# Optimization experiments

Measured on AMD Instinct MI355X. Metric: run time of the kernel, lower is better.

## Reference

```python
import jax, jax.numpy as jnp
import numpy as np

KR = 2  # nb_row == stride_row
KC = 2  # nb_col == stride_col


def setup_inputs() -> dict:
    key = jax.random.key(0)
    k1, k2, k3 = jax.random.split(key, 3)
    B, C, H, W_ = 32, 32, 128, 128
    F = 64
    OR, OC = H // KR, W_ // KC
    x = jax.random.normal(k1, (B, C, H, W_), dtype=jnp.float32)
    W = jax.random.normal(k2, (F, C, H, W_), dtype=jnp.float32) * 0.05
    b = jax.random.normal(k3, (OR, OC, F), dtype=jnp.float32) * 0.05
    return {"x": x, "W": W, "b": b}


def reference(x, W, b):
    # x: (B, C, H, W), W: (F, C, H, W) -- unshared per-pixel weights
    # per-pixel channel contraction: (B, F, H, W)
    out = jnp.einsum('bchw,fchw->bfhw', x, W)
    B, F, H, Wd = out.shape
    OR, OC = H // KR, Wd // KC
    # stride*avg_pool == exact sum over non-overlapping (KR, KC) patches
    out = out.reshape(B, F, OR, KR, OC, KC).sum(axis=(3, 5))
    # keras does a RAW reshape of b from (OR, OC, F) to (1, F, OR, OC)
    out = out + b.reshape(1, F, OR, OC)
    return jax.nn.relu(out)
```

## Files before the change

kernel.cpp:

```cpp
#include <hip/hip_runtime.h>
#include <stdint.h>


#define CC  32
#define HH  128
#define WWD 128
#define FF  64
#define ORR 64
#define OCC 64
#define NIT 32
#define HW  (HH * WWD)
#define CHW (CC * HH * WWD)

__global__ __launch_bounds__(512, 4) void lc2d_kernel(
    const float* __restrict__ x, const float* __restrict__ wgt,
    const float* __restrict__ bias, float* __restrict__ out)
{
    __shared__ __align__(16) float Xs[4][2048];
    __shared__ __align__(16) float Ws[4][2048];

    const int tid  = threadIdx.x;
    const int id   = blockIdx.x;
    const int fblk = id >> 8;
    const int low  = id & 255;
    const int oct = ((low & 1) << 1) | (low >> 7);
    const int orr = (low >> 1) & 63;
    const int w0  = oct * 32;
    const int h0  = orr * 2;

    const int lane = tid & 63;
    const int wv   = tid >> 6;
    const int chk  = lane & 7;
    const int sub  = lane >> 3;

    const int r  = wv * 8 + sub;
    const int sr = r >> 5;
    const int br = r & 31;
    const float* gx = x   + (((br * CC) * HH) + h0 + sr) * WWD + w0 + chk * 4;
    const float* gw = wgt + ((((fblk * 32 + br) * CC) * HH) + h0 + sr) * WWD + w0 + chk * 4;

    auto issue = [&](int p) {
        __builtin_amdgcn_global_load_lds(
            (const __attribute__((address_space(1))) void*)gx,
            (__attribute__((address_space(3))) void*)(&Xs[p][wv * 256]), 16, 0, 0);
        __builtin_amdgcn_global_load_lds(
            (const __attribute__((address_space(1))) void*)gw,
            (__attribute__((address_space(3))) void*)(&Ws[p][wv * 256]), 16, 0, 0);
        gx += HW; gw += HW;
    };

    const int ocg = tid & 7;
    const int bg  = (tid >> 3) & 7;
    const int xoff = bg * 128 + ocg * 4;
    const int woff = wv * 128 + ocg * 4;

    float acc0[4][4], acc1[4][4];
#pragma unroll
    for (int i = 0; i < 4; ++i)
#pragma unroll
        for (int q = 0; q < 4; ++q) { acc0[i][q] = 0.f; acc1[i][q] = 0.f; }

    issue(0); issue(1); issue(2); issue(3);

    for (int it = 0; it < NIT; ++it) {
        const int rem = NIT - 1 - it;
        if (rem >= 3)      asm volatile("s_waitcnt vmcnt(6)");
        else if (rem == 2) asm volatile("s_waitcnt vmcnt(4)");
        else if (rem == 1) asm volatile("s_waitcnt vmcnt(2)");
        else               asm volatile("s_waitcnt vmcnt(0)");
        __builtin_amdgcn_sched_barrier(0);
        __builtin_amdgcn_s_barrier();
        __builtin_amdgcn_sched_barrier(0);

        const int p = it & 3;
        const float* Xp = Xs[p];
        const float* Wp = Ws[p];
#pragma unroll
        for (int s = 0; s < 2; ++s) {
            const float4* xr = (const float4*)(Xp + s * 1024 + xoff);
            const float4* wr = (const float4*)(Wp + s * 1024 + woff);
            float4 xa[4], wb[4];
#pragma unroll
            for (int i = 0; i < 4; ++i) xa[i] = xr[i * 8];
#pragma unroll
            for (int q = 0; q < 4; ++q) wb[q] = wr[q * 8];
#pragma unroll
            for (int i = 0; i < 4; ++i)
#pragma unroll
                for (int q = 0; q < 4; ++q) {
                    acc0[i][q] = fmaf(xa[i].x, wb[q].x, acc0[i][q]);
                    acc0[i][q] = fmaf(xa[i].y, wb[q].y, acc0[i][q]);
                    acc1[i][q] = fmaf(xa[i].z, wb[q].z, acc1[i][q]);
                    acc1[i][q] = fmaf(xa[i].w, wb[q].w, acc1[i][q]);
                }
        }
        __builtin_amdgcn_sched_barrier(0);
        __builtin_amdgcn_s_barrier();
        __builtin_amdgcn_sched_barrier(0);
        if (it + 4 < NIT) issue(p);
    }

    const int oc0 = oct * 16 + ocg * 2;
#pragma unroll
    for (int q = 0; q < 4; ++q) {
        const int f = fblk * 32 + wv * 4 + q;
        const float2 bv = *(const float2*)(bias + f * (ORR * OCC) + orr * OCC + oc0);
#pragma unroll
        for (int i = 0; i < 4; ++i) {
            const int b = bg * 4 + i;
            float2 o;
            o.x = fmaxf(acc0[i][q] + bv.x, 0.f);
            o.y = fmaxf(acc1[i][q] + bv.y, 0.f);
            *(float2*)(out + (((b * FF + f) * ORR + orr) * OCC) + oc0) = o;
        }
    }
}

extern "C" void kernel_launch(void* const* d_in, const int* in_sizes, int n_in,
                              void* d_out, int out_size, void* d_ws, size_t ws_size,
                              hipStream_t stream) {
    (void)in_sizes; (void)n_in; (void)d_ws; (void)ws_size; (void)out_size;
    const float* x    = (const float*)d_in[0];
    const float* wgt  = (const float*)d_in[1];
    const float* bias = (const float*)d_in[2];
    float* out        = (float*)d_out;
    lc2d_kernel<<<dim3(512, 1, 1), dim3(512, 1, 1), 0, stream>>>(x, wgt, bias, out);
}
```

Measured before the change: 263.4 us.

## Load weights directly into registers instead of staging through LDS

Weights are no longer staged in shared memory. Each thread loads its own weight float4s straight from global memory into double-buffered registers, prefetching the next channel while computing the current one, and only the activations still go through the async global-to-LDS pipeline. This halves LDS traffic and footprint and removes the LDS reads for weights, since each weight element is used by only one thread group. The cost is more VGPRs and hand-tuned vmcnt wait counts, which must exactly match the number of outstanding loads. If the compiler reorders or merges those loads, the counts can become wrong.

```diff
diff --git a/kernel.cpp b/kernel.cpp
--- a/kernel.cpp
+++ b/kernel.cpp
@@ -12,12 +12,13 @@
 #define HW  (HH * WWD)
 #define CHW (CC * HH * WWD)
 
+#define SB() __builtin_amdgcn_sched_barrier(0)
+
 __global__ __launch_bounds__(512, 4) void lc2d_kernel(
     const float* __restrict__ x, const float* __restrict__ wgt,
     const float* __restrict__ bias, float* __restrict__ out)
 {
     __shared__ __align__(16) float Xs[4][2048];
-    __shared__ __align__(16) float Ws[4][2048];
 
     const int tid  = threadIdx.x;
     const int id   = blockIdx.x;
@@ -33,26 +34,21 @@
     const int chk  = lane & 7;
     const int sub  = lane >> 3;
 
-    const int r  = wv * 8 + sub;
-    const int sr = r >> 5;
-    const int br = r & 31;
-    const float* gx = x   + (((br * CC) * HH) + h0 + sr) * WWD + w0 + chk * 4;
-    const float* gw = wgt + ((((fblk * 32 + br) * CC) * HH) + h0 + sr) * WWD + w0 + chk * 4;
+    const int r = wv * 8 + sub;
+    const float* gx = x + ((((r & 31) * CC) * HH) + h0 + (r >> 5)) * WWD + w0 + chk * 4;
 
-    auto issue = [&](int p) {
+    auto issueX = [&](int p) {
         __builtin_amdgcn_global_load_lds(
             (const __attribute__((address_space(1))) void*)gx,
             (__attribute__((address_space(3))) void*)(&Xs[p][wv * 256]), 16, 0, 0);
-        __builtin_amdgcn_global_load_lds(
-            (const __attribute__((address_space(1))) void*)gw,
-            (__attribute__((address_space(3))) void*)(&Ws[p][wv * 256]), 16, 0, 0);
-        gx += HW; gw += HW;
+        gx += HW;
     };
 
     const int ocg = tid & 7;
     const int bg  = (tid >> 3) & 7;
     const int xoff = bg * 128 + ocg * 4;
-    const int woff = wv * 128 + ocg * 4;
+
+    const float* wp = wgt + (size_t)(fblk * 32 + wv * 4) * CHW + (size_t)h0 * WWD + w0 + ocg * 4;
 
     float acc0[4][4], acc1[4][4];
 #pragma unroll
@@ -60,45 +56,79 @@
 #pragma unroll
         for (int q = 0; q < 4; ++q) { acc0[i][q] = 0.f; acc1[i][q] = 0.f; }
 
-    issue(0); issue(1); issue(2); issue(3);
+    issueX(0); issueX(1); issueX(2); issueX(3);
+    SB();
+    float4 wEs0[4], wEs1[4], wOs0[4], wOs1[4];
+#pragma unroll
+    for (int q = 0; q < 4; ++q) wEs0[q] = *(const float4*)(wp + q * CHW);
+#pragma unroll
+    for (int q = 0; q < 4; ++q) wEs1[q] = *(const float4*)(wp + q * CHW + WWD);
+    SB();
+    const float* wnx = wp + HW;
 
-    for (int it = 0; it < NIT; ++it) {
-        const int rem = NIT - 1 - it;
-        if (rem >= 3)      asm volatile("s_waitcnt vmcnt(6)");
-        else if (rem == 2) asm volatile("s_waitcnt vmcnt(4)");
-        else if (rem == 1) asm volatile("s_waitcnt vmcnt(2)");
-        else               asm volatile("s_waitcnt vmcnt(0)");
-        __builtin_amdgcn_sched_barrier(0);
-        __builtin_amdgcn_s_barrier();
-        __builtin_amdgcn_sched_barrier(0);
+#define CHUNK(IT, CS0, CS1, NS0, NS1)                                           \
+    {                                                                           \
+        const int it_ = (IT);                                                   \
+        if (it_ == 0)      asm volatile("s_waitcnt vmcnt(11)");                 \
+        else if (it_ == 1) asm volatile("s_waitcnt vmcnt(19)");                 \
+        else               asm volatile("s_waitcnt vmcnt(24)");                 \
+        SB();                                                                   \
+        __builtin_amdgcn_s_barrier();        \
+        SB();                                                                   \
+        if (it_ + 1 < NIT) {                        \
+            _Pragma("unroll")                                                   \
+            for (int q = 0; q < 4; ++q) NS0[q] = *(const float4*)(wnx + q * CHW); \
+        }                                                                       \
+        SB();                                                                   \
+        const float* Xp = &Xs[it_ & 3][0];                                      \
+        {                                                            \
+            const float4* xr = (const float4*)(Xp + xoff);                      \
+            float4 xa[4];                                                       \
+            _Pragma("unroll")                                                   \
+            for (int i = 0; i < 4; ++i) xa[i] = xr[i * 8];                      \
+            _Pragma("unroll")                                                   \
+            for (int i = 0; i < 4; ++i)                                         \
+                _Pragma("unroll")                                               \
+                for (int q = 0; q < 4; ++q) {                                   \
+                    acc0[i][q] = fmaf(xa[i].x, CS0[q].x, acc0[i][q]);           \
+                    acc0[i][q] = fmaf(xa[i].y, CS0[q].y, acc0[i][q]);           \
+                    acc1[i][q] = fmaf(xa[i].z, CS0[q].z, acc1[i][q]);           \
+                    acc1[i][q] = fmaf(xa[i].w, CS0[q].w, acc1[i][q]);           \
+                }                                                               \
+        }                                                                       \
+        SB();                                                                   \
+        if (it_ + 1 < NIT) {                        \
+            _Pragma("unroll")                                                   \
+            for (int q = 0; q < 4; ++q) NS1[q] = *(const float4*)(wnx + q * CHW + WWD); \
+        }                                                                       \
+        SB();                                                                   \
+        {                                                            \
+            const float4* xr = (const float4*)(Xp + 1024 + xoff);               \
+            float4 xa[4];                                                       \
+            _Pragma("unroll")                                                   \
+            for (int i = 0; i < 4; ++i) xa[i] = xr[i * 8];                      \
+            _Pragma("unroll")                                                   \
+            for (int i = 0; i < 4; ++i)                                         \
+                _Pragma("unroll")                                               \
+                for (int q = 0; q < 4; ++q) {                                   \
+                    acc0[i][q] = fmaf(xa[i].x, CS1[q].x, acc0[i][q]);           \
+                    acc0[i][q] = fmaf(xa[i].y, CS1[q].y, acc0[i][q]);           \
+                    acc1[i][q] = fmaf(xa[i].z, CS1[q].z, acc1[i][q]);           \
+                    acc1[i][q] = fmaf(xa[i].w, CS1[q].w, acc1[i][q]);           \
+                }                                                               \
+        }                                                                       \
+        SB();                                                                   \
+        __builtin_amdgcn_s_barrier();                \
+        SB();                                                                   \
+        if (it_ + 4 < NIT) issueX(it_ & 3);             \
+        wnx += HW;                                                              \
+    }
 
-        const int p = it & 3;
-        const float* Xp = Xs[p];
-        const float* Wp = Ws[p];
-#pragma unroll
-        for (int s = 0; s < 2; ++s) {
-            const float4* xr = (const float4*)(Xp + s * 1024 + xoff);
-            const float4* wr = (const float4*)(Wp + s * 1024 + woff);
-            float4 xa[4], wb[4];
-#pragma unroll
-            for (int i = 0; i < 4; ++i) xa[i] = xr[i * 8];
-#pragma unroll
-            for (int q = 0; q < 4; ++q) wb[q] = wr[q * 8];
-#pragma unroll
-            for (int i = 0; i < 4; ++i)
-#pragma unroll
-                for (int q = 0; q < 4; ++q) {
-                    acc0[i][q] = fmaf(xa[i].x, wb[q].x, acc0[i][q]);
-                    acc0[i][q] = fmaf(xa[i].y, wb[q].y, acc0[i][q]);
-                    acc1[i][q] = fmaf(xa[i].z, wb[q].z, acc1[i][q]);
-                    acc1[i][q] = fmaf(xa[i].w, wb[q].w, acc1[i][q]);
-                }
-        }
-        __builtin_amdgcn_sched_barrier(0);
-        __builtin_amdgcn_s_barrier();
-        __builtin_amdgcn_sched_barrier(0);
-        if (it + 4 < NIT) issue(p);
+    for (int ih = 0; ih < NIT / 2; ++ih) {
+        CHUNK(2 * ih,     wEs0, wEs1, wOs0, wOs1);
+        CHUNK(2 * ih + 1, wOs0, wOs1, wEs0, wEs1);
     }
+#undef CHUNK
 
     const int oc0 = oct * 16 + ocg * 2;
 #pragma unroll
```

After: 759.7 us. 2.88x slower.
